# Kernel tuning notes

Measured on AMD Instinct MI355X. Metric: run time of the kernel, lower is better.

## Reference

```python
import jax, jax.numpy as jnp
import numpy as np

B, H, W, C = 32, 56, 56, 192
WS, SH = 7, 3            # window size, shift size
NH = 6                   # num heads
HD = C // NH             # head dim = 32
N = WS * WS              # tokens per window = 49
NW = (H // WS) * (W // WS)  # windows per image = 64
HID = int(C * 4.0)       # MLP hidden = 768
EPS = 1e-6               # flax LayerNorm default


def _rel_index():
    # (N, N) int index into the (2*WS-1)^2 relative position bias table
    coords = np.stack(np.meshgrid(np.arange(WS), np.arange(WS), indexing='ij')).reshape(2, -1)
    rel = coords[:, :, None] - coords[:, None, :]          # (2, N, N)
    rel = rel.transpose(1, 2, 0) + (WS - 1)                # shift to >= 0
    idx = rel[..., 0] * (2 * WS - 1) + rel[..., 1]
    return jnp.asarray(idx, jnp.int32)


def _attn_mask():
    # standard Swin shifted-window mask: -100 between different regions
    img = np.zeros((H, W))
    cnt = 0
    for hs in (slice(0, -WS), slice(-WS, -SH), slice(-SH, None)):
        for ws in (slice(0, -WS), slice(-WS, -SH), slice(-SH, None)):
            img[hs, ws] = cnt
            cnt += 1
    win = img.reshape(H // WS, WS, W // WS, WS).transpose(0, 2, 1, 3).reshape(NW, N)
    diff = win[:, None, :] - win[:, :, None]
    return jnp.asarray(np.where(diff != 0, -100.0, 0.0), jnp.float32)


def setup_inputs() -> dict:
    key = jax.random.key(0)
    ks = jax.random.split(key, 8)
    s = 0.02
    return {
        'x': jax.random.normal(ks[0], (B, H, W, C), jnp.float32),
        'mask': _attn_mask(),
        'rel_index': _rel_index(),
        'ln1_scale': jnp.ones((C,), jnp.float32),
        'ln1_bias': jnp.zeros((C,), jnp.float32),
        'qkv_w': jax.random.normal(ks[1], (C, 3 * C), jnp.float32) * s,
        'qkv_b': jnp.zeros((3 * C,), jnp.float32),
        'rpb_table': jax.random.normal(ks[2], ((2 * WS - 1) ** 2, NH), jnp.float32) * s,
        'proj_w': jax.random.normal(ks[3], (C, C), jnp.float32) * s,
        'proj_b': jnp.zeros((C,), jnp.float32),
        'ln2_scale': jnp.ones((C,), jnp.float32),
        'ln2_bias': jnp.zeros((C,), jnp.float32),
        'mlp_w1': jax.random.normal(ks[4], (C, HID), jnp.float32) * s,
        'mlp_b1': jnp.zeros((HID,), jnp.float32),
        'mlp_w2': jax.random.normal(ks[5], (HID, C), jnp.float32) * s,
        'mlp_b2': jnp.zeros((C,), jnp.float32),
    }


def _ln(x, scale, bias):
    mu = jnp.mean(x, axis=-1, keepdims=True)
    var = jnp.mean(jnp.square(x - mu), axis=-1, keepdims=True)
    return (x - mu) * jax.lax.rsqrt(var + EPS) * scale + bias


def reference(x, mask, rel_index, ln1_scale, ln1_bias, qkv_w, qkv_b, rpb_table,
              proj_w, proj_b, ln2_scale, ln2_bias, mlp_w1, mlp_b1, mlp_w2, mlp_b2):
    # ---- W-MSA branch ----
    y = _ln(x, ln1_scale, ln1_bias)
    # cyclic shift (grid divisible by window -> pad_to_blocks is a no-op)
    y = jnp.roll(y, shift=(-SH, -SH), axis=(1, 2))
    # window partition: (B,H,W,C) -> (B*NW, N, C)
    y = y.reshape(B, H // WS, WS, W // WS, WS, C).transpose(0, 1, 3, 2, 4, 5)
    y = y.reshape(B * NW, N, C)
    # qkv: (B*NW, N, 3, NH, HD) -> q,k,v each (B*NW, NH, N, HD)
    qkv = (y @ qkv_w + qkv_b).reshape(B * NW, N, 3, NH, HD).transpose(2, 0, 3, 1, 4)
    q, k, v = qkv[0], qkv[1], qkv[2]
    attn = jnp.einsum('bhnd,bhmd->bhnm', q, k) * (HD ** -0.5)
    # relative position bias: (N,N,NH) -> (1,NH,N,N)
    attn = attn + rpb_table[rel_index].transpose(2, 0, 1)[None]
    # shifted-window mask: broadcast over batch and heads
    attn = attn.reshape(B, NW, NH, N, N) + mask[None, :, None]
    attn = jax.nn.softmax(attn.reshape(B * NW, NH, N, N), axis=-1)
    y = jnp.einsum('bhnm,bhmd->bhnd', attn, v).transpose(0, 2, 1, 3).reshape(B * NW, N, C)
    y = y @ proj_w + proj_b
    # window reverse and un-shift
    y = y.reshape(B, H // WS, W // WS, WS, WS, C).transpose(0, 1, 3, 2, 4, 5).reshape(B, H, W, C)
    y = jnp.roll(y, shift=(SH, SH), axis=(1, 2))
    x = x + y
    # ---- MLP branch ----
    z = _ln(x, ln2_scale, ln2_bias)
    z = jax.nn.gelu(z @ mlp_w1 + mlp_b1)  # flax nn.gelu default (tanh approx)
    z = z @ mlp_w2 + mlp_b2
    return x + z
```

## Files before the change

kernel.cpp:

```cpp
#include <hip/hip_runtime.h>


typedef __bf16 bf16_t;
typedef __bf16 bf16x8 __attribute__((ext_vector_type(8)));
typedef float  f32x4  __attribute__((ext_vector_type(4)));

__device__ inline float wred_sum(float v) {
#pragma unroll
  for (int o = 32; o; o >>= 1) v += __shfl_xor(v, o);
  return v;
}

__device__ inline float gelu_tanh(float x) {
  float u = 0.7978845608028654f * (x + 0.044715f * x * x * x);
  float e = __expf(2.f * u);
  float t = 1.f - 2.f / (e + 1.f);
  return 0.5f * x * (1.f + t);
}

__global__ __launch_bounds__(256) void k_ln1_win(
    const float* __restrict__ x, const float* __restrict__ sc,
    const float* __restrict__ bi, bf16_t* __restrict__ yw, int b0, int nTok) {
  int wv = (int)((blockIdx.x * 256 + threadIdx.x) >> 6);
  int lane = threadIdx.x & 63;
  if (wv >= nTok) return;
  int winL = wv / 49;
  int t = wv - winL * 49;
  int wi = winL & 63;
  int b = b0 + (winL >> 6);
  int t7 = t / 7;
  int hr = (wi >> 3) * 7 + t7;
  int wr = (wi & 7) * 7 + (t - t7 * 7);
  int h = hr + 3; if (h >= 56) h -= 56;
  int w = wr + 3; if (w >= 56) w -= 56;
  const float* xp = x + (((size_t)(b * 56 + h)) * 56 + w) * 192;
  float v0 = xp[lane], v1 = xp[lane + 64], v2 = xp[lane + 128];
  float s = wred_sum(v0 + v1 + v2);
  float q = wred_sum(v0 * v0 + v1 * v1 + v2 * v2);
  float mu = s * (1.f / 192.f);
  float var = q * (1.f / 192.f) - mu * mu;
  float rs = rsqrtf(var + 1e-6f);
  bf16_t* op = yw + (size_t)wv * 192;
  op[lane]       = (bf16_t)((v0 - mu) * rs * sc[lane]       + bi[lane]);
  op[lane + 64]  = (bf16_t)((v1 - mu) * rs * sc[lane + 64]  + bi[lane + 64]);
  op[lane + 128] = (bf16_t)((v2 - mu) * rs * sc[lane + 128] + bi[lane + 128]);
}

__global__ __launch_bounds__(256) void k_transpose_cvt(
    const float* __restrict__ in, bf16_t* __restrict__ out, int K, int N) {
  int idx = blockIdx.x * 256 + threadIdx.x;
  if (idx >= K * N) return;
  int n = idx / K, k = idx - n * K;
  out[idx] = (bf16_t)in[(size_t)k * N + n];
}

__global__ __launch_bounds__(256) void k_rpb(
    const int* __restrict__ relidx, const float* __restrict__ rpb,
    float* __restrict__ rpbh) {
  int idx = blockIdx.x * 256 + threadIdx.x;
  if (idx >= 6 * 2401) return;
  int h = idx / 2401, n = idx - h * 2401;
  rpbh[idx] = rpb[relidx[n] * 6 + h];
}

template <int K>
__global__ __launch_bounds__(256, 2) void k_gemm_bs(
    const bf16_t* __restrict__ A, const bf16_t* __restrict__ Bt,
    const float* __restrict__ bias, bf16_t* __restrict__ C, int Nn, int nMt) {
  constexpr int NKS = K / 32;
  int tid = threadIdx.x;
  int w = tid >> 6, lane = tid & 63;
  int c = lane & 15, g = lane >> 4;
  int bn = blockIdx.x;
  bf16x8 bf[4][NKS];
  const bf16_t* bp = Bt + (size_t)(bn * 64 + c) * K + 8 * g;
#pragma unroll
  for (int jc = 0; jc < 4; ++jc)
#pragma unroll
    for (int ks = 0; ks < NKS; ++ks)
      bf[jc][ks] = *(const bf16x8*)(bp + (size_t)jc * 16 * K + 32 * ks);
  float4 bias4[4];
#pragma unroll
  for (int jc = 0; jc < 4; ++jc)
    bias4[jc] = *(const float4*)(bias + bn * 64 + jc * 16 + 4 * g);
  for (int mt = blockIdx.y; mt < nMt; mt += gridDim.y) {
    int m0 = mt * 256 + w * 64;
    f32x4 acc[4][4] = {};
    const bf16_t* ap = A + (size_t)(m0 + c) * K + 8 * g;
#pragma unroll
    for (int ks = 0; ks < NKS; ++ks) {
      bf16x8 af[4];
#pragma unroll
      for (int ir = 0; ir < 4; ++ir)
        af[ir] = *(const bf16x8*)(ap + (size_t)ir * 16 * K + 32 * ks);
#pragma unroll
      for (int jc = 0; jc < 4; ++jc)
#pragma unroll
        for (int ir = 0; ir < 4; ++ir)
          acc[jc][ir] = __builtin_amdgcn_mfma_f32_16x16x32_bf16(
              bf[jc][ks], af[ir], acc[jc][ir], 0, 0, 0);
    }
#pragma unroll
    for (int ir = 0; ir < 4; ++ir) {
      bf16_t* cp = C + (size_t)(m0 + ir * 16 + c) * Nn + bn * 64 + 4 * g;
#pragma unroll
      for (int jc = 0; jc < 4; ++jc) {
        union { uint2 u; bf16_t e[4]; } pk;
#pragma unroll
        for (int r = 0; r < 4; ++r)
          pk.e[r] = (bf16_t)(acc[jc][ir][r] + ((const float*)&bias4[jc])[r]);
        *(uint2*)(cp + jc * 16) = pk.u;
      }
    }
  }
}

__global__ __launch_bounds__(64) void k_attn(
    const bf16_t* __restrict__ qkv, const float* __restrict__ rpbh,
    const float* __restrict__ mask, bf16_t* __restrict__ attn_out) {
  __shared__ char sm[12288];
  int blk = blockIdx.x;
  int wL = blk / 6, h = blk - wL * 6;
  int lane = threadIdx.x;
  int c = lane & 15, g = lane >> 4;
  const bf16_t* baseq = qkv + (size_t)wL * (49 * 576);

  {
    const float* mw = mask + (size_t)(wL & 63) * 2401;
    const float* bh = rpbh + (size_t)h * 2401;
    __bf16* bl = (__bf16*)sm;
    for (int idx = lane; idx < 2401; idx += 64)
      bl[idx] = (__bf16)(bh[idx] + mw[idx]);
  }

  char* vts = sm + 8192;
  {
    uint4 z4 = {0u, 0u, 0u, 0u};
#pragma unroll
    for (int it = 0; it < 4; ++it)
      *(uint4*)(vts + lane * 16 + it * 1024) = z4;
#pragma unroll
    for (int it = 0; it < 4; ++it) {
      int task = lane + 64 * it;
      if (task < 196) {
        int m = task % 49, dc = task / 49;
        union { bf16x8 v; __bf16 e[8]; } u;
        u.v = *(const bf16x8*)(baseq + (size_t)m * 576 + 384 + h * 32 + dc * 8);
#pragma unroll
        for (int e0 = 0; e0 < 8; ++e0) {
          int d = dc * 8 + e0;
          *(__bf16*)(vts + d * 128 + ((2 * m) ^ ((d & 7) << 4))) = u.e[e0];
        }
      }
    }
  }

  f32x4 s[4][4] = {};
  bf16x8 qf[4], kf[4];
#pragma unroll
  for (int i = 0; i < 4; ++i) {
    int n = c + 16 * i; if (n > 48) n = 48;
    qf[i] = *(const bf16x8*)(baseq + (size_t)n * 576 + h * 32 + g * 8);
  }
#pragma unroll
  for (int j = 0; j < 4; ++j) {
    int m = c + 16 * j; if (m > 48) m = 48;
    kf[j] = *(const bf16x8*)(baseq + (size_t)m * 576 + 192 + h * 32 + g * 8);
  }
#pragma unroll
  for (int i = 0; i < 4; ++i)
#pragma unroll
    for (int j = 0; j < 4; ++j)
      s[i][j] = __builtin_amdgcn_mfma_f32_16x16x32_bf16(qf[i], kf[j], s[i][j],
                                                        0, 0, 0);

  const __bf16* bl = (const __bf16*)sm;
  float mxv[4][4], sum[4][4];
#pragma unroll
  for (int i = 0; i < 4; ++i)
#pragma unroll
    for (int r = 0; r < 4; ++r) {
      int n = 16 * i + 4 * g + r;
      int nc = n > 48 ? 48 : n;
      float best = -1e30f;
#pragma unroll
      for (int j = 0; j < 4; ++j) {
        int m = 16 * j + c;
        float v = -1e30f;
        if (m < 49)
          v = s[i][j][r] * 0.17677669529663687f + (float)bl[nc * 49 + m];
        s[i][j][r] = v;
        best = fmaxf(best, v);
      }
      mxv[i][r] = best;
    }
#pragma unroll
  for (int o = 8; o; o >>= 1)
#pragma unroll
    for (int i = 0; i < 4; ++i)
#pragma unroll
      for (int r = 0; r < 4; ++r)
        mxv[i][r] = fmaxf(mxv[i][r], __shfl_xor(mxv[i][r], o));
#pragma unroll
  for (int i = 0; i < 4; ++i)
#pragma unroll
    for (int r = 0; r < 4; ++r) {
      float ss = 0.f;
#pragma unroll
      for (int j = 0; j < 4; ++j) {
        float p = __expf(s[i][j][r] - mxv[i][r]);
        s[i][j][r] = p;
        ss += p;
      }
      sum[i][r] = ss;
    }
#pragma unroll
  for (int o = 8; o; o >>= 1)
#pragma unroll
    for (int i = 0; i < 4; ++i)
#pragma unroll
      for (int r = 0; r < 4; ++r)
        sum[i][r] += __shfl_xor(sum[i][r], o);

#pragma unroll
  for (int i = 0; i < 4; ++i)
#pragma unroll
    for (int j = 0; j < 4; ++j)
#pragma unroll
      for (int r = 0; r < 4; ++r) {
        int n = 16 * i + 4 * g + r;
        int m = 16 * j + c;
        int offb = n * 128 + ((2 * m) ^ ((n & 7) << 4));
        *(__bf16*)(sm + offb) = (__bf16)s[i][j][r];
      }

  f32x4 o2[4][2] = {};
#pragma unroll
  for (int kt = 0; kt < 2; ++kt) {
    bf16x8 pf[4], vf[2];
#pragma unroll
    for (int i = 0; i < 4; ++i) {
      int n = c + 16 * i;
      int cb = (16 * g + 64 * kt) ^ ((n & 7) << 4);
      pf[i] = *(const bf16x8*)(sm + n * 128 + cb);
    }
#pragma unroll
    for (int dt = 0; dt < 2; ++dt) {
      int d = c + 16 * dt;
      vf[dt] = *(const bf16x8*)(vts + d * 128 +
                                ((64 * kt + 16 * g) ^ ((d & 7) << 4)));
    }
#pragma unroll
    for (int i = 0; i < 4; ++i)
#pragma unroll
      for (int dt = 0; dt < 2; ++dt)
        o2[i][dt] = __builtin_amdgcn_mfma_f32_16x16x32_bf16(pf[i], vf[dt],
                                                            o2[i][dt], 0, 0, 0);
  }

#pragma unroll
  for (int i = 0; i < 4; ++i)
#pragma unroll
    for (int dt = 0; dt < 2; ++dt)
#pragma unroll
      for (int r = 0; r < 4; ++r) {
        int n = 16 * i + 4 * g + r;
        if (n < 49) {
          int d = 16 * dt + c;
          attn_out[((size_t)wL * 49 + n) * 192 + h * 32 + d] =
              (bf16_t)(o2[i][dt][r] / sum[i][r]);
        }
      }
}

__global__ __launch_bounds__(256) void k_unwin_ln2(
    const float* __restrict__ x, const bf16_t* __restrict__ projw,
    const float* __restrict__ sc, const float* __restrict__ bi,
    float* __restrict__ out, bf16_t* __restrict__ z, int b0, int nTok) {
  int wv = (int)((blockIdx.x * 256 + threadIdx.x) >> 6);
  int lane = threadIdx.x & 63;
  if (wv >= nTok) return;
  int bL = wv / 3136;
  int rem = wv - bL * 3136;
  int hh = rem / 56, ww2 = rem - hh * 56;
  int b = b0 + bL;
  int hr = hh + 53; if (hr >= 56) hr -= 56;
  int wr = ww2 + 53; if (wr >= 56) wr -= 56;
  int winL = bL * 64 + (hr / 7) * 8 + (wr / 7);
  int t = (hr % 7) * 7 + (wr % 7);
  const bf16_t* pp = projw + ((size_t)winL * 49 + t) * 192;
  size_t gtok = ((size_t)(b * 56 + hh)) * 56 + ww2;
  const float* xp = x + gtok * 192;
  float v0 = xp[lane]       + (float)pp[lane];
  float v1 = xp[lane + 64]  + (float)pp[lane + 64];
  float v2 = xp[lane + 128] + (float)pp[lane + 128];
  float* op = out + gtok * 192;
  op[lane] = v0; op[lane + 64] = v1; op[lane + 128] = v2;
  float s = wred_sum(v0 + v1 + v2);
  float q = wred_sum(v0 * v0 + v1 * v1 + v2 * v2);
  float mu = s * (1.f / 192.f);
  float var = q * (1.f / 192.f) - mu * mu;
  float rs = rsqrtf(var + 1e-6f);
  bf16_t* zp = z + gtok * 192;
  zp[lane]       = (bf16_t)((v0 - mu) * rs * sc[lane]       + bi[lane]);
  zp[lane + 64]  = (bf16_t)((v1 - mu) * rs * sc[lane + 64]  + bi[lane + 64]);
  zp[lane + 128] = (bf16_t)((v2 - mu) * rs * sc[lane + 128] + bi[lane + 128]);
}

__global__ __launch_bounds__(256, 2) void k_mlp_fused3(
    const bf16_t* __restrict__ z, const bf16_t* __restrict__ w1T,
    const float* __restrict__ b1, const bf16_t* __restrict__ w2T,
    const float* __restrict__ b2, float* __restrict__ out) {
  __shared__ char hsm[32768];
  int tid = threadIdx.x;
  int wv = tid >> 6, lane = tid & 63;
  int c = lane & 15, g = lane >> 4;
  char* wbase = hsm + wv * 8192;
  int row0 = blockIdx.x * 128 + wv * 32;

  bf16x8 zfr[2][6];
  const bf16_t* zp = z + (size_t)(row0 + c) * 192 + 8 * g;
#pragma unroll
  for (int ir = 0; ir < 2; ++ir)
#pragma unroll
    for (int ks = 0; ks < 6; ++ks)
      zfr[ir][ks] = *(const bf16x8*)(zp + (size_t)ir * 16 * 192 + 32 * ks);

  f32x4 acc2[12][2] = {};

#pragma unroll 2
  for (int hc = 0; hc < 12; ++hc) {
    char* hbuf = wbase + (hc & 1) * 4096;
    f32x4 acc1[4][2] = {};
    const bf16_t* w1p = w1T + (size_t)(hc * 64 + c) * 192 + 8 * g;
#pragma unroll
    for (int ks = 0; ks < 6; ++ks) {
      bf16x8 wf[4];
#pragma unroll
      for (int jh = 0; jh < 4; ++jh)
        wf[jh] = *(const bf16x8*)(w1p + (size_t)jh * 16 * 192 + 32 * ks);
#pragma unroll
      for (int jh = 0; jh < 4; ++jh)
#pragma unroll
        for (int ir = 0; ir < 2; ++ir)
          acc1[jh][ir] = __builtin_amdgcn_mfma_f32_16x16x32_bf16(
              wf[jh], zfr[ir][ks], acc1[jh][ir], 0, 0, 0);
    }
    const bf16_t* w2p = w2T + (size_t)c * 768 + hc * 64 + 8 * g;
    bf16x8 wf2a[12];
#pragma unroll
    for (int jc = 0; jc < 12; ++jc)
      wf2a[jc] = *(const bf16x8*)(w2p + (size_t)jc * 16 * 768);
#pragma unroll
    for (int jh = 0; jh < 4; ++jh) {
      float4 b1v = *(const float4*)(b1 + hc * 64 + jh * 16 + 4 * g);
#pragma unroll
      for (int ir = 0; ir < 2; ++ir) {
        union { uint2 u; __bf16 e[4]; } pk;
#pragma unroll
        for (int r = 0; r < 4; ++r)
          pk.e[r] = (__bf16)gelu_tanh(acc1[jh][ir][r] + ((const float*)&b1v)[r]);
        int rl = ir * 16 + c;
        *(uint2*)(hbuf + rl * 128 + ((32 * jh + 8 * g) ^ ((rl & 7) << 4))) =
            pk.u;
      }
    }
    {
      bf16x8 af[2];
#pragma unroll
      for (int ir = 0; ir < 2; ++ir) {
        int rl = ir * 16 + c;
        af[ir] = *(const bf16x8*)(hbuf + rl * 128 +
                                  ((16 * g) ^ ((rl & 7) << 4)));
      }
#pragma unroll
      for (int jc = 0; jc < 12; ++jc)
#pragma unroll
        for (int ir = 0; ir < 2; ++ir)
          acc2[jc][ir] = __builtin_amdgcn_mfma_f32_16x16x32_bf16(
              wf2a[jc], af[ir], acc2[jc][ir], 0, 0, 0);
    }
    {
      bf16x8 wf2b[12];
#pragma unroll
      for (int jc = 0; jc < 12; ++jc)
        wf2b[jc] = *(const bf16x8*)(w2p + (size_t)jc * 16 * 768 + 32);
      bf16x8 af[2];
#pragma unroll
      for (int ir = 0; ir < 2; ++ir) {
        int rl = ir * 16 + c;
        af[ir] = *(const bf16x8*)(hbuf + rl * 128 +
                                  ((64 + 16 * g) ^ ((rl & 7) << 4)));
      }
#pragma unroll
      for (int jc = 0; jc < 12; ++jc)
#pragma unroll
        for (int ir = 0; ir < 2; ++ir)
          acc2[jc][ir] = __builtin_amdgcn_mfma_f32_16x16x32_bf16(
              wf2b[jc], af[ir], acc2[jc][ir], 0, 0, 0);
    }
  }
#pragma unroll
  for (int jc = 0; jc < 12; ++jc) {
    float4 b2v = *(const float4*)(b2 + jc * 16 + 4 * g);
#pragma unroll
    for (int ir = 0; ir < 2; ++ir) {
      int row = row0 + ir * 16 + c;
      float* op = out + (size_t)row * 192 + jc * 16 + 4 * g;
      float4 cur = *(float4*)op;
      cur.x += acc2[jc][ir][0] + b2v.x;
      cur.y += acc2[jc][ir][1] + b2v.y;
      cur.z += acc2[jc][ir][2] + b2v.z;
      cur.w += acc2[jc][ir][3] + b2v.w;
      *(float4*)op = cur;
    }
  }
}

extern "C" void kernel_launch(void* const* d_in, const int* in_sizes, int n_in,
                              void* d_out, int out_size, void* d_ws,
                              size_t ws_size, hipStream_t stream) {
  (void)in_sizes; (void)n_in; (void)out_size;
  const float* x     = (const float*)d_in[0];
  const float* maskp = (const float*)d_in[1];
  const int*   reli  = (const int*)d_in[2];
  const float* ln1s  = (const float*)d_in[3];
  const float* ln1b  = (const float*)d_in[4];
  const float* qkvw  = (const float*)d_in[5];
  const float* qkvb  = (const float*)d_in[6];
  const float* rpb   = (const float*)d_in[7];
  const float* projw = (const float*)d_in[8];
  const float* projb = (const float*)d_in[9];
  const float* ln2s  = (const float*)d_in[10];
  const float* ln2b  = (const float*)d_in[11];
  const float* w1    = (const float*)d_in[12];
  const float* b1    = (const float*)d_in[13];
  const float* w2    = (const float*)d_in[14];
  const float* b2    = (const float*)d_in[15];
  float* out = (float*)d_out;

  auto aup = [](size_t v) { return (v + 255) & ~(size_t)255; };
  char* base = (char*)d_ws;
  size_t off = 0;
  bf16_t* z_buf = (bf16_t*)(base + off); off += aup((size_t)100352 * 192 * 2);
  bf16_t* qkvT  = (bf16_t*)(base + off); off += aup((size_t)576 * 192 * 2);
  bf16_t* projT = (bf16_t*)(base + off); off += aup((size_t)192 * 192 * 2);
  bf16_t* w1T   = (bf16_t*)(base + off); off += aup((size_t)768 * 192 * 2);
  bf16_t* w2T   = (bf16_t*)(base + off); off += aup((size_t)192 * 768 * 2);
  float*  rpbh  = (float*)(base + off);  off += aup((size_t)6 * 2401 * 4);
  size_t offB = off;

  int Bc = 32;
  while (Bc > 4 && offB + (size_t)Bc * 3136 * (576 + 192) * 2 > ws_size)
    Bc >>= 1;
  bf16_t* bufB = (bf16_t*)(base + offB);
  bf16_t* bufA = (bf16_t*)(base + offB + aup((size_t)Bc * 3136 * 576 * 2));

  k_transpose_cvt<<<(192 * 576 + 255) / 256, 256, 0, stream>>>(qkvw, qkvT, 192, 576);
  k_transpose_cvt<<<(192 * 192 + 255) / 256, 256, 0, stream>>>(projw, projT, 192, 192);
  k_transpose_cvt<<<(192 * 768 + 255) / 256, 256, 0, stream>>>(w1, w1T, 192, 768);
  k_transpose_cvt<<<(768 * 192 + 255) / 256, 256, 0, stream>>>(w2, w2T, 768, 192);
  k_rpb<<<(6 * 2401 + 255) / 256, 256, 0, stream>>>(reli, rpb, rpbh);

  for (int b0 = 0; b0 < 32; b0 += Bc) {
    int nTok = Bc * 3136, nWin = Bc * 64;
    int nMt = nTok / 256;
    k_ln1_win<<<nTok / 4, 256, 0, stream>>>(x, ln1s, ln1b, bufA, b0, nTok);
    {
      int nbn = 576 / 64;
      int gy = (512 + nbn - 1) / nbn; if (gy > nMt) gy = nMt;
      k_gemm_bs<192><<<dim3(nbn, gy), 256, 0, stream>>>(bufA, qkvT, qkvb, bufB,
                                                        576, nMt);
    }
    k_attn<<<nWin * 6, 64, 0, stream>>>(bufB, rpbh, maskp, bufA);
    {
      int nbn = 192 / 64;
      int gy = (512 + nbn - 1) / nbn; if (gy > nMt) gy = nMt;
      k_gemm_bs<192><<<dim3(nbn, gy), 256, 0, stream>>>(bufA, projT, projb,
                                                        bufB, 192, nMt);
    }
    k_unwin_ln2<<<nTok / 4, 256, 0, stream>>>(x, bufB, ln2s, ln2b, out, z_buf,
                                              b0, nTok);
  }

  k_mlp_fused3<<<100352 / 128, 256, 0, stream>>>(z_buf, w1T, b1, w2T, b2, out);
}
```

Before: 787.7 us.

## Stage MLP weight chunks in shared memory with register prefetch

The fused MLP kernel now cooperatively loads each 64-wide hidden chunk of w1 and w2 into swizzled LDS once per block, instead of having every wave read weights directly from global memory. The next chunk is prefetched into registers while the current one is computed. This cuts redundant global and L2 weight traffic across the four waves. In exchange it adds two block barriers per chunk and raises LDS use to 64KB per block, which may limit occupancy.

```diff
diff --git a/kernel.cpp b/kernel.cpp
--- a/kernel.cpp
+++ b/kernel.cpp
@@ -124,7 +124,6 @@
   int lane = threadIdx.x;
   int c = lane & 15, g = lane >> 4;
   const bf16_t* baseq = qkv + (size_t)wL * (49 * 576);
-
   {
     const float* mw = mask + (size_t)(wL & 63) * 2401;
     const float* bh = rpbh + (size_t)h * 2401;
@@ -132,7 +131,6 @@
     for (int idx = lane; idx < 2401; idx += 64)
       bl[idx] = (__bf16)(bh[idx] + mw[idx]);
   }
-
   char* vts = sm + 8192;
   {
     uint4 z4 = {0u, 0u, 0u, 0u};
@@ -154,7 +152,6 @@
       }
     }
   }
-
   f32x4 s[4][4] = {};
   bf16x8 qf[4], kf[4];
 #pragma unroll
@@ -173,7 +170,6 @@
     for (int j = 0; j < 4; ++j)
       s[i][j] = __builtin_amdgcn_mfma_f32_16x16x32_bf16(qf[i], kf[j], s[i][j],
                                                         0, 0, 0);
-
   const __bf16* bl = (const __bf16*)sm;
   float mxv[4][4], sum[4][4];
 #pragma unroll
@@ -221,7 +217,6 @@
 #pragma unroll
       for (int r = 0; r < 4; ++r)
         sum[i][r] += __shfl_xor(sum[i][r], o);
-
 #pragma unroll
   for (int i = 0; i < 4; ++i)
 #pragma unroll
@@ -233,7 +228,6 @@
         int offb = n * 128 + ((2 * m) ^ ((n & 7) << 4));
         *(__bf16*)(sm + offb) = (__bf16)s[i][j][r];
       }
-
   f32x4 o2[4][2] = {};
 #pragma unroll
   for (int kt = 0; kt < 2; ++kt) {
@@ -257,7 +251,6 @@
         o2[i][dt] = __builtin_amdgcn_mfma_f32_16x16x32_bf16(pf[i], vf[dt],
                                                             o2[i][dt], 0, 0, 0);
   }
-
 #pragma unroll
   for (int i = 0; i < 4; ++i)
 #pragma unroll
@@ -307,15 +300,17 @@
   zp[lane + 128] = (bf16_t)((v2 - mu) * rs * sc[lane + 128] + bi[lane + 128]);
 }
 
-__global__ __launch_bounds__(256, 2) void k_mlp_fused3(
+__global__ __launch_bounds__(256, 2) void k_mlp_fused4(
     const bf16_t* __restrict__ z, const bf16_t* __restrict__ w1T,
     const float* __restrict__ b1, const bf16_t* __restrict__ w2T,
     const float* __restrict__ b2, float* __restrict__ out) {
-  __shared__ char hsm[32768];
+  __shared__ char w1s[24576];
+  __shared__ char w2s[24576];
+  __shared__ char hsm[16384];
   int tid = threadIdx.x;
   int wv = tid >> 6, lane = tid & 63;
   int c = lane & 15, g = lane >> 4;
-  char* wbase = hsm + wv * 8192;
+  char* hbuf = hsm + wv * 4096;
   int row0 = blockIdx.x * 128 + wv * 32;
 
   bf16x8 zfr[2][6];
@@ -326,19 +321,53 @@
     for (int ks = 0; ks < 6; ++ks)
       zfr[ir][ks] = *(const bf16x8*)(zp + (size_t)ir * 16 * 192 + 32 * ks);
 
+  uint4 sv1[6], sv2[6];
+  int r1[6], s1[6], r2[6], s2[6];
+#pragma unroll
+  for (int i = 0; i < 6; ++i) {
+    int t = tid + 256 * i;
+    r1[i] = t / 24; s1[i] = t - r1[i] * 24;
+    r2[i] = t >> 3; s2[i] = t & 7;
+  }
+#pragma unroll
+  for (int i = 0; i < 6; ++i)
+    sv1[i] = *(const uint4*)(w1T + (size_t)r1[i] * 192 + s1[i] * 8);
+#pragma unroll
+  for (int i = 0; i < 6; ++i)
+    sv2[i] = *(const uint4*)(w2T + (size_t)r2[i] * 768 + s2[i] * 8);
+
   f32x4 acc2[12][2] = {};
 
-#pragma unroll 2
   for (int hc = 0; hc < 12; ++hc) {
-    char* hbuf = wbase + (hc & 1) * 4096;
+#pragma unroll
+    for (int i = 0; i < 6; ++i)
+      *(uint4*)(w1s + r1[i] * 384 + ((s1[i] * 16) ^ ((r1[i] & 7) << 4))) =
+          sv1[i];
+#pragma unroll
+    for (int i = 0; i < 6; ++i)
+      *(uint4*)(w2s + r2[i] * 128 + ((s2[i] * 16) ^ ((r2[i] & 7) << 4))) =
+          sv2[i];
+    __syncthreads();
+    if (hc + 1 < 12) {
+      const bf16_t* w1n = w1T + (size_t)(hc + 1) * 64 * 192;
+#pragma unroll
+      for (int i = 0; i < 6; ++i)
+        sv1[i] = *(const uint4*)(w1n + (size_t)r1[i] * 192 + s1[i] * 8);
+      const bf16_t* w2n = w2T + (size_t)(hc + 1) * 64;
+#pragma unroll
+      for (int i = 0; i < 6; ++i)
+        sv2[i] = *(const uint4*)(w2n + (size_t)r2[i] * 768 + s2[i] * 8);
+    }
     f32x4 acc1[4][2] = {};
-    const bf16_t* w1p = w1T + (size_t)(hc * 64 + c) * 192 + 8 * g;
 #pragma unroll
     for (int ks = 0; ks < 6; ++ks) {
       bf16x8 wf[4];
 #pragma unroll
-      for (int jh = 0; jh < 4; ++jh)
-        wf[jh] = *(const bf16x8*)(w1p + (size_t)jh * 16 * 192 + 32 * ks);
+      for (int jh = 0; jh < 4; ++jh) {
+        int hcol = jh * 16 + c;
+        wf[jh] = *(const bf16x8*)(w1s + hcol * 384 +
+                                  ((64 * ks + 16 * g) ^ ((c & 7) << 4)));
+      }
 #pragma unroll
       for (int jh = 0; jh < 4; ++jh)
 #pragma unroll
@@ -346,11 +375,6 @@
           acc1[jh][ir] = __builtin_amdgcn_mfma_f32_16x16x32_bf16(
               wf[jh], zfr[ir][ks], acc1[jh][ir], 0, 0, 0);
     }
-    const bf16_t* w2p = w2T + (size_t)c * 768 + hc * 64 + 8 * g;
-    bf16x8 wf2a[12];
-#pragma unroll
-    for (int jc = 0; jc < 12; ++jc)
-      wf2a[jc] = *(const bf16x8*)(w2p + (size_t)jc * 16 * 768);
 #pragma unroll
     for (int jh = 0; jh < 4; ++jh) {
       float4 b1v = *(const float4*)(b1 + hc * 64 + jh * 16 + 4 * g);
@@ -365,40 +389,27 @@
             pk.u;
       }
     }
-    {
+#pragma unroll
+    for (int ks2 = 0; ks2 < 2; ++ks2) {
       bf16x8 af[2];
 #pragma unroll
       for (int ir = 0; ir < 2; ++ir) {
         int rl = ir * 16 + c;
         af[ir] = *(const bf16x8*)(hbuf + rl * 128 +
-                                  ((16 * g) ^ ((rl & 7) << 4)));
-      }
-#pragma unroll
-      for (int jc = 0; jc < 12; ++jc)
+                                  ((64 * ks2 + 16 * g) ^ ((rl & 7) << 4)));
+      }
+#pragma unroll
+      for (int jc = 0; jc < 12; ++jc) {
+        int oc = jc * 16 + c;
+        bf16x8 wf2 = *(const bf16x8*)(w2s + oc * 128 +
+                                      ((64 * ks2 + 16 * g) ^ ((c & 7) << 4)));
 #pragma unroll
         for (int ir = 0; ir < 2; ++ir)
           acc2[jc][ir] = __builtin_amdgcn_mfma_f32_16x16x32_bf16(
-              wf2a[jc], af[ir], acc2[jc][ir], 0, 0, 0);
-    }
-    {
-      bf16x8 wf2b[12];
-#pragma unroll
-      for (int jc = 0; jc < 12; ++jc)
-        wf2b[jc] = *(const bf16x8*)(w2p + (size_t)jc * 16 * 768 + 32);
-      bf16x8 af[2];
-#pragma unroll
-      for (int ir = 0; ir < 2; ++ir) {
-        int rl = ir * 16 + c;
-        af[ir] = *(const bf16x8*)(hbuf + rl * 128 +
-                                  ((64 + 16 * g) ^ ((rl & 7) << 4)));
-      }
-#pragma unroll
-      for (int jc = 0; jc < 12; ++jc)
-#pragma unroll
-        for (int ir = 0; ir < 2; ++ir)
-          acc2[jc][ir] = __builtin_amdgcn_mfma_f32_16x16x32_bf16(
-              wf2b[jc], af[ir], acc2[jc][ir], 0, 0, 0);
-    }
+              wf2, af[ir], acc2[jc][ir], 0, 0, 0);
+      }
+    }
+    __syncthreads();
   }
 #pragma unroll
   for (int jc = 0; jc < 12; ++jc) {
@@ -483,5 +494,5 @@
                                               b0, nTok);
   }
 
-  k_mlp_fused3<<<100352 / 128, 256, 0, stream>>>(z_buf, w1T, b1, w2T, b2, out);
-}
+  k_mlp_fused4<<<100352 / 128, 256, 0, stream>>>(z_buf, w1T, b1, w2T, b2, out);
+}
```

After: 698.4 us. 11.3% less time.
